# Optimization experiments

Hardware: AMD Instinct MI355X
Metric: run time of the kernel (lower is better)

The kernel has to match this reference:

```python
import jax, jax.numpy as jnp
import numpy as np

D_MODEL = 1024
NHEAD = 16
HEAD_DIM = D_MODEL // NHEAD
EPS = 1e-8


def setup_inputs() -> dict:
    key = jax.random.key(0)
    ks = jax.random.split(key, 10)
    B, T = 2, 2048
    s = 1.0 / np.sqrt(D_MODEL)
    return {
        "query": jax.random.normal(ks[0], (B, T, D_MODEL), jnp.float32),
        "key": jax.random.normal(ks[1], (B, T, D_MODEL), jnp.float32),
        "value": jax.random.normal(ks[2], (B, T, D_MODEL), jnp.float32),
        "frac": jax.random.uniform(ks[3], (B, T), jnp.float32),
        "Wq": jax.random.normal(ks[4], (D_MODEL, D_MODEL), jnp.float32) * s,
        "bq": jnp.zeros((D_MODEL,), jnp.float32),
        "Wk": jax.random.normal(ks[5], (D_MODEL, D_MODEL), jnp.float32) * s,
        "bk": jnp.zeros((D_MODEL,), jnp.float32),
        "Wv": jax.random.normal(ks[6], (D_MODEL, D_MODEL), jnp.float32) * s,
        "bv": jnp.zeros((D_MODEL,), jnp.float32),
        "attn_bias": jax.random.normal(ks[7], (HEAD_DIM,), jnp.float32) * 0.02,
        "Wo": jax.random.normal(ks[8], (D_MODEL, D_MODEL), jnp.float32) * s,
        "bo": jnpp if False else jnp.zeros((D_MODEL,), jnp.float32),
    }


def reference(query, key, value, frac, Wq, bq, Wk, bk, Wv, bv, attn_bias, Wo, bo):
    B, T, _ = query.shape
    H, Dh = NHEAD, HEAD_DIM
    scale = Dh ** -0.5

    # torch Linear: x @ W.T + b
    Q = (query @ Wq.T + bq).reshape(B, T, H, Dh).transpose(0, 2, 1, 3)  # [B,H,T,Dh]
    K = (key @ Wk.T + bk).reshape(B, T, H, Dh).transpose(0, 2, 1, 3)
    V = (value @ Wv.T + bv).reshape(B, T, H, Dh).transpose(0, 2, 1, 3)

    # factor_ij = (frac_j - frac_i) / (frac_i*frac_j + eps), shape [B,T,T]
    fi = frac[:, :, None]
    fj = frac[:, None, :]
    factor = (fj - fi) / (fi * fj + EPS)

    # sum_d (Q_i*K_j + attn_bias*factor)_d == QK^T + sum(attn_bias)*factor
    bias_sum = jnp.sum(attn_bias)
    logits = jnp.einsum('bhid,bhjd->bhij', Q, K) + bias_sum * factor[:, None, :, :]
    logits = logits * scale

    probs = jax.nn.softmax(logits, axis=-1)  # dropout p=0.0 (eval)
    out = jnp.einsum('bhij,bhjd->bhid', probs, V)  # [B,H,T,Dh]
    out = out.transpose(0, 2, 1, 3).reshape(B, T, H * Dh)
    return out @ Wo.T + bo
```

## Files before the change

kernel.cpp:

```cpp
#include <hip/hip_runtime.h>

typedef short s16x8 __attribute__((ext_vector_type(8)));
typedef float f32x4 __attribute__((ext_vector_type(4)));
typedef unsigned int u32x2 __attribute__((ext_vector_type(2)));
typedef unsigned short u16;
typedef unsigned int u32;

#define D_MODEL 1024
#define NHEAD   16
#define HD      64
#define TSEQ    2048
#define NB      2
#define MROWS   4096
#define NSPLIT  2
#define NTILES  (TSEQ / 64 / NSPLIT)

#define LOG2E 1.4426950408889634f
#define QSCALE (0.125f * LOG2E)

__device__ __forceinline__ u16 f2bf(float f) {
  unsigned u = __builtin_bit_cast(unsigned, f);
  u += 0x7fffu + ((u >> 16) & 1u);
  return (u16)(u >> 16);
}

__device__ __forceinline__ float bf2f(u16 x) {
  return __builtin_bit_cast(float, (u32)x << 16);
}

__device__ __forceinline__ u32 cvtpk(float lo, float hi) {
  u32 r;
  asm("v_cvt_pk_bf16_f32 %0, %1, %2" : "=v"(r) : "v"(lo), "v"(hi));
  return r;
}

__device__ __forceinline__ float exp2fast(float x) {
#if __has_builtin(__builtin_amdgcn_exp2f)
  return __builtin_amdgcn_exp2f(x);
#else
  return exp2f(x);
#endif
}

__device__ __forceinline__ float rcpfast(float x) {
#if __has_builtin(__builtin_amdgcn_rcpf)
  return __builtin_amdgcn_rcpf(x);
#else
  return 1.f / x;
#endif
}

__device__ __forceinline__ void gload16(const void* g, void* l) {
  __builtin_amdgcn_global_load_lds((const __attribute__((address_space(1))) void*)g,
                                   (__attribute__((address_space(3))) void*)l,
                                   16, 0, 0);
}

__global__ void cvt_all(const float* __restrict__ q, const float* __restrict__ k,
                        const float* __restrict__ v, const float* __restrict__ wq,
                        const float* __restrict__ wk, const float* __restrict__ wv,
                        const float* __restrict__ wo, const float* __restrict__ ab,
                        u16* qb, u16* kb, u16* vb, u16* wqb, u16* wkb, u16* wvb, u16* wob,
                        float* bsum) {
  if (blockIdx.x == 16384) {
    if (threadIdx.x < 64) {
      float s = ab[threadIdx.x];
#pragma unroll
      for (int m = 32; m >= 1; m >>= 1) s += __shfl_xor(s, m);
      if (threadIdx.x == 0) bsum[0] = s * 0.125f * LOG2E;
    }
    return;
  }
  int i = blockIdx.x * 256 + threadIdx.x;
  const float* src; u16* dst; int off;
  if (i < 3 * 1048576) {
    int t = i >> 20; off = i & 1048575;
    src = (t == 0) ? q : (t == 1) ? k : v;
    dst = (t == 0) ? qb : (t == 1) ? kb : vb;
  } else {
    int j = i - 3 * 1048576;
    int t = j >> 18; off = j & 262143;
    src = (t == 0) ? wq : (t == 1) ? wk : (t == 2) ? wv : wo;
    dst = (t == 0) ? wqb : (t == 1) ? wkb : (t == 2) ? wvb : wob;
  }
  float4 x = ((const float4*)src)[off];
  ushort4 o;
  o.x = f2bf(x.x); o.y = f2bf(x.y); o.z = f2bf(x.z); o.w = f2bf(x.w);
  ((ushort4*)dst)[off] = o;
}

template <int BM, int BN, int WN>
__device__ __forceinline__ void gemm_core(const u16* __restrict__ A, const u16* __restrict__ Bt,
                                          const float* __restrict__ bias, void* __restrict__ out,
                                          float oscale, int mode, u16* lds) {
  constexpr int K = 1024, N = 1024;
  constexpr int WM = 4 / WN;
  constexpr int WTM = BM / WM, WTN = BN / WN;
  constexpr int MR = WTM / 16, NR = WTN / 16;
  constexpr int ASZ = BM * 32, BSZ = BN * 32;
  constexpr int AISS = ASZ / 2048, BISS = BSZ / 2048;
  u16* lA = lds;
  u16* lB = lds + 2 * ASZ;

  const int tid = threadIdx.x;
  const int wid = tid >> 6, lane = tid & 63;
  const int l15 = lane & 15, lgp = lane >> 4;
  const int wr = wid / WN, wc = wid % WN;
  const int m0 = blockIdx.y * BM, n0 = blockIdx.x * BN;

  const u16* gA[AISS];
  const u16* gB[BISS];
#pragma unroll
  for (int i = 0; i < AISS; ++i) {
    int tp = i * 256 + tid, row = tp % BM, kc = tp / BM;
    gA[i] = A + (size_t)(m0 + row) * K + kc * 8;
  }
#pragma unroll
  for (int i = 0; i < BISS; ++i) {
    int tp = i * 256 + tid, row = tp % BN, kc = tp / BN;
    gB[i] = Bt + (size_t)(n0 + row) * K + kc * 8;
  }

  f32x4 acc[MR][NR];
#pragma unroll
  for (int m = 0; m < MR; ++m)
#pragma unroll
    for (int n = 0; n < NR; ++n) acc[m][n] = (f32x4){0.f, 0.f, 0.f, 0.f};

  auto stage = [&](int buf, int k0) {
#pragma unroll
    for (int i = 0; i < AISS; ++i)
      gload16(gA[i] + k0, lA + buf * ASZ + (i * 256 + tid) * 8);
#pragma unroll
    for (int i = 0; i < BISS; ++i)
      gload16(gB[i] + k0, lB + buf * BSZ + (i * 256 + tid) * 8);
  };

  int cur = 0;
  stage(0, 0);
  __syncthreads();
  for (int k0 = 0; k0 < K; k0 += 32) {
    if (k0 + 32 < K) stage(cur ^ 1, k0 + 32);
    const u16* a = lA + cur * ASZ;
    const u16* b = lB + cur * BSZ;
    s16x8 af[MR], bf[NR];
#pragma unroll
    for (int m = 0; m < MR; ++m)
      af[m] = *(const s16x8*)(a + lgp * BM * 8 + (wr * WTM + m * 16 + l15) * 8);
#pragma unroll
    for (int n = 0; n < NR; ++n)
      bf[n] = *(const s16x8*)(b + lgp * BN * 8 + (wc * WTN + n * 16 + l15) * 8);
    __builtin_amdgcn_s_setprio(1);
#pragma unroll
    for (int m = 0; m < MR; ++m)
#pragma unroll
      for (int n = 0; n < NR; ++n)
        acc[m][n] = __builtin_amdgcn_mfma_f32_16x16x32_bf16(af[m], bf[n], acc[m][n], 0, 0, 0);
    __builtin_amdgcn_s_setprio(0);
    __syncthreads();
    cur ^= 1;
  }

  float bvv[NR];
#pragma unroll
  for (int n = 0; n < NR; ++n) bvv[n] = bias[n0 + wc * WTN + n * 16 + l15];

#pragma unroll
  for (int m = 0; m < MR; ++m) {
    int rowb = m0 + wr * WTM + m * 16 + lgp * 4;
#pragma unroll
    for (int n = 0; n < NR; ++n) {
      int col = n0 + wc * WTN + n * 16 + l15;
#pragma unroll
      for (int r = 0; r < 4; ++r) {
        int row = rowb + r;
        float vv = (acc[m][n][r] + bvv[n]) * oscale;
        if (mode == 2) {
          ((float*)out)[(size_t)row * N + col] = vv;
        } else {
          int b = row >> 11, t = row & 2047;
          int h = col >> 6, d = col & 63;
          u16 x = f2bf(vv);
          if (mode == 0)
            ((u16*)out)[(((size_t)(b * NHEAD + h) * TSEQ + t) << 6) + d] = x;
          else
            ((u16*)out)[(((size_t)(b * NHEAD + h) * HD + d) << 11) + t] = x;
        }
      }
    }
  }
}

__global__ __launch_bounds__(256) void gemm_qkv(const u16* __restrict__ qb, const u16* __restrict__ kb,
                                                const u16* __restrict__ vb,
                                                const u16* __restrict__ Wqb, const u16* __restrict__ Wkb,
                                                const u16* __restrict__ Wvb,
                                                const float* __restrict__ bq, const float* __restrict__ bk,
                                                const float* __restrict__ bv,
                                                u16* Qp, u16* Kp, u16* Vtp) {
  __shared__ __align__(16) u16 lds[2 * 128 * 32 * 2];
  int z = blockIdx.z;
  const u16* A  = (z == 0) ? qb : (z == 1) ? kb : vb;
  const u16* Bt = (z == 0) ? Wqb : (z == 1) ? Wkb : Wvb;
  const float* bias = (z == 0) ? bq : (z == 1) ? bk : bv;
  u16* out = (z == 0) ? Qp : (z == 1) ? Kp : Vtp;
  int mode = (z == 2) ? 1 : 0;
  float oscale = (z == 0) ? QSCALE : 1.0f;
  gemm_core<128, 128, 2>(A, Bt, bias, out, oscale, mode, lds);
}

__global__ __launch_bounds__(256) void gemm_out(const u16* __restrict__ A, const u16* __restrict__ Bt,
                                                const float* __restrict__ bias, float* __restrict__ out) {
  __shared__ __align__(16) u16 lds[2 * 64 * 32 + 2 * 128 * 32];
  gemm_core<64, 128, 4>(A, Bt, bias, out, 1.0f, 2, lds);
}

__global__ __launch_bounds__(256, 4) void attn_kernel(const u16* __restrict__ Qp,
                                                      const u16* __restrict__ Kp,
                                                      const u16* __restrict__ Vt,
                                                      const float* __restrict__ frac,
                                                      const float* __restrict__ bsum,
                                                      u16* __restrict__ o0,
                                                      u16* __restrict__ o1,
                                                      float2* __restrict__ ml) {
  __shared__ __align__(16) u16 kbuf[64 * 64];
  __shared__ __align__(16) u16 vbuf[2][64 * 64];
  __shared__ __align__(16) u16 plds[4][16 * 64];
  const int tid = threadIdx.x, wid = tid >> 6, lane = tid & 63;
  const int l15 = lane & 15, lgp = lane >> 4;
  const int bh = blockIdx.y, b = bh >> 4, h = bh & 15;
  const int z = blockIdx.z;
  const int kvbase = z * (TSEQ / NSPLIT);
  u16* opart = z ? o1 : o0;
  float2* mlz = ml + z * (NB * NHEAD * TSEQ);
  const u16* Qh = Qp + (size_t)bh * TSEQ * HD;
  const u16* Kh = Kp + (size_t)bh * TSEQ * HD;
  const u16* Vh = Vt + (size_t)bh * HD * TSEQ;
  const float* fb = frac + b * TSEQ;
  const float bs = bsum[0];
  const float THR2 = 24.0f;
  const int q0 = blockIdx.x * 64 + wid * 16;

  const int srow = lane >> 3;
  const int sg8 = ((lane & 7) ^ srow) * 8;
  const int rbase = wid * 8 + srow;

  const int ofs0 = l15 * 64 + ((lgp ^ (l15 & 7)) * 8);
  const int ofs1 = l15 * 64 + (((4 + lgp) ^ (l15 & 7)) * 8);

  s16x8 qf[2];
#pragma unroll
  for (int ks = 0; ks < 2; ++ks)
    qf[ks] = *(const s16x8*)(Qh + (size_t)(q0 + l15) * HD + ks * 32 + lgp * 8);

  const float fi = fb[q0 + l15];
  const float nbfi = -bs * fi;
  float m2run = -1e30f;
  float lsum = 0.f;
  f32x4 o[4];
#pragma unroll
  for (int nd = 0; nd < 4; ++nd) o[nd] = (f32x4){0.f, 0.f, 0.f, 0.f};

  auto stageK = [&](int t) {
    int kv0s = kvbase + t * 64;
#pragma unroll
    for (int i = 0; i < 2; ++i)
      gload16(Kh + (size_t)(kv0s + i * 32 + rbase) * HD + sg8, &kbuf[i * 2048 + wid * 512]);
  };
  auto stageV = [&](int buf, int t) {
    int kv0s = kvbase + t * 64;
#pragma unroll
    for (int i = 0; i < 2; ++i)
      gload16(Vh + (size_t)(i * 32 + rbase) * TSEQ + kv0s + sg8, &vbuf[buf][i * 2048 + wid * 512]);
  };

  int cur = 0;
  stageK(0);
  stageV(0, 0);
  __syncthreads();

  for (int t = 0; t < NTILES; ++t) {
    s16x8 kf[4][2];
#pragma unroll
    for (int n = 0; n < 4; ++n) {
      kf[n][0] = *(const s16x8*)(&kbuf[0] + n * 1024 + ofs0);
      kf[n][1] = *(const s16x8*)(&kbuf[0] + n * 1024 + ofs1);
    }
    float4 fj4[4];
#pragma unroll
    for (int n = 0; n < 4; ++n)
      fj4[n] = *(const float4*)(fb + kvbase + t * 64 + n * 16 + lgp * 4);

    __syncthreads();
    if (t + 1 < NTILES) { stageK(t + 1); stageV(cur ^ 1, t + 1); }

    f32x4 s[4];
    __builtin_amdgcn_s_setprio(1);
#pragma unroll
    for (int n = 0; n < 4; ++n) {
      f32x4 a = (f32x4){0.f, 0.f, 0.f, 0.f};
      a = __builtin_amdgcn_mfma_f32_16x16x32_bf16(kf[n][0], qf[0], a, 0, 0, 0);
      a = __builtin_amdgcn_mfma_f32_16x16x32_bf16(kf[n][1], qf[1], a, 0, 0, 0);
      s[n] = a;
    }
    __builtin_amdgcn_s_setprio(0);

    float pmax = -1e30f;
#pragma unroll
    for (int n = 0; n < 4; ++n) {
#pragma unroll
      for (int r = 0; r < 4; ++r) {
        float fj = (r == 0) ? fj4[n].x : (r == 1) ? fj4[n].y : (r == 2) ? fj4[n].z : fj4[n].w;
        float num = __builtin_fmaf(bs, fj, nbfi);
        float den = __builtin_fmaf(fi, fj, 1e-8f);
        float l2 = __builtin_fmaf(num, rcpfast(den), s[n][r]);
        s[n][r] = l2;
        pmax = fmaxf(pmax, l2);
      }
    }

    if (__any((pmax - m2run) > THR2)) {
      float tm = fmaxf(pmax, __shfl_xor(pmax, 16));
      tm = fmaxf(tm, __shfl_xor(tm, 32));
      float m2n = fmaxf(m2run, tm);
      float alpha = exp2fast(m2run - m2n);
      lsum *= alpha;
      m2run = m2n;
      float af[4];
#pragma unroll
      for (int r = 0; r < 4; ++r) af[r] = __shfl(alpha, lgp * 4 + r);
#pragma unroll
      for (int nd = 0; nd < 4; ++nd)
#pragma unroll
        for (int r = 0; r < 4; ++r) o[nd][r] *= af[r];
    }

    u32 w[4][2];
    {
      float ps = 0.f;
#pragma unroll
      for (int n = 0; n < 4; ++n) {
#pragma unroll
        for (int s2 = 0; s2 < 2; ++s2) {
          float p0 = exp2fast(s[n][2 * s2 + 0] - m2run);
          float p1 = exp2fast(s[n][2 * s2 + 1] - m2run);
          ps += p0 + p1;
          w[n][s2] = cvtpk(p0, p1);
        }
      }
      lsum += ps;
    }

    u16* pw = &plds[wid][0];
#pragma unroll
    for (int n = 0; n < 4; ++n) {
      int idx = l15 * 64 + ((n * 16 + lgp * 4) ^ ((l15 & 7) << 3));
      *(u32x2*)(pw + idx) = (u32x2){w[n][0], w[n][1]};
    }
    s16x8 pf[2];
#pragma unroll
    for (int ks = 0; ks < 2; ++ks) {
      int idx = l15 * 64 + ((ks * 32 + lgp * 8) ^ ((l15 & 7) << 3));
      pf[ks] = *(const s16x8*)(pw + idx);
    }

    const u16* vbp = &vbuf[cur][0];
    __builtin_amdgcn_s_setprio(1);
#pragma unroll
    for (int nd = 0; nd < 4; ++nd) {
      s16x8 vf0 = *(const s16x8*)(vbp + nd * 1024 + ofs0);
      s16x8 vf1 = *(const s16x8*)(vbp + nd * 1024 + ofs1);
      o[nd] = __builtin_amdgcn_mfma_f32_16x16x32_bf16(pf[0], vf0, o[nd], 0, 0, 0);
      o[nd] = __builtin_amdgcn_mfma_f32_16x16x32_bf16(pf[1], vf1, o[nd], 0, 0, 0);
    }
    __builtin_amdgcn_s_setprio(0);

    __syncthreads();
    cur ^= 1;
  }

  {
    float l = lsum;
    l += __shfl_xor(l, 16);
    l += __shfl_xor(l, 32);
    if (lgp == 0)
      mlz[(bh << 11) + q0 + l15] = make_float2(m2run, l);
#pragma unroll
    for (int nd = 0; nd < 4; ++nd)
#pragma unroll
      for (int r = 0; r < 4; ++r) {
        int q = q0 + lgp * 4 + r;
        opart[((size_t)(b * TSEQ + q)) * D_MODEL + h * HD + nd * 16 + l15] = f2bf(o[nd][r]);
      }
  }
}

__global__ __launch_bounds__(256) void attn_combine(const u16* __restrict__ o0,
                                                    const u16* __restrict__ o1,
                                                    const float2* __restrict__ ml,
                                                    u16* __restrict__ aout) {
  int g = blockIdx.x * 256 + threadIdx.x;
  int bth = g >> 3, j0 = (g & 7) * 8;
  int b = bth >> 15, t = (bth >> 4) & 2047, h = bth & 15;
  int mlidx = (((b << 4) | h) << 11) | t;
  float2 v0 = ml[mlidx];
  float2 v1 = ml[NB * NHEAD * TSEQ + mlidx];
  float M = fmaxf(v0.x, v1.x);
  float a0 = exp2fast(v0.x - M), a1 = exp2fast(v1.x - M);
  float rd = __fdividef(1.f, __builtin_fmaf(v0.y, a0, v1.y * a1));
  float s0 = a0 * rd, s1 = a1 * rd;
  size_t base = (size_t)bth * 64 + j0;
  s16x8 x0 = *(const s16x8*)(o0 + base);
  s16x8 x1 = *(const s16x8*)(o1 + base);
  s16x8 out;
#pragma unroll
  for (int j = 0; j < 8; ++j) {
    float f = __builtin_fmaf(bf2f((u16)x0[j]), s0, bf2f((u16)x1[j]) * s1);
    out[j] = (short)f2bf(f);
  }
  *(s16x8*)(aout + base) = out;
}

extern "C" void kernel_launch(void* const* d_in, const int* in_sizes, int n_in,
                              void* d_out, int out_size, void* d_ws, size_t ws_size,
                              hipStream_t stream) {
  const float* query = (const float*)d_in[0];
  const float* key_  = (const float*)d_in[1];
  const float* value = (const float*)d_in[2];
  const float* frac  = (const float*)d_in[3];
  const float* Wq    = (const float*)d_in[4];
  const float* bq    = (const float*)d_in[5];
  const float* Wk    = (const float*)d_in[6];
  const float* bk    = (const float*)d_in[7];
  const float* Wv    = (const float*)d_in[8];
  const float* bv    = (const float*)d_in[9];
  const float* abias = (const float*)d_in[10];
  const float* Wo    = (const float*)d_in[11];
  const float* bo    = (const float*)d_in[12];

  char* ws = (char*)d_ws;
  size_t off = 0;
  auto alloc = [&](size_t bytes) { char* p = ws + off; off += (bytes + 255) & ~255ULL; return p; };
  const size_t XB = (size_t)MROWS * D_MODEL * 2;
  const size_t WB = (size_t)D_MODEL * D_MODEL * 2;
  u16* qb  = (u16*)alloc(XB);
  u16* kb  = (u16*)alloc(XB);
  u16* vb  = (u16*)alloc(XB);
  u16* Wqb = (u16*)alloc(WB);
  u16* Wkb = (u16*)alloc(WB);
  u16* Wvb = (u16*)alloc(WB);
  u16* Wob = (u16*)alloc(WB);
  float* bsum = (float*)alloc(256);
  u16* Qp  = (u16*)alloc(XB);
  u16* Kp  = (u16*)alloc(XB);
  u16* Vtp = (u16*)alloc(XB);
  u16* AO  = (u16*)alloc(XB);

  u16* o0 = qb;
  u16* o1 = kb;
  float2* ml = (float2*)vb;

  cvt_all<<<dim3(16385), dim3(256), 0, stream>>>(query, key_, value, Wq, Wk, Wv, Wo, abias,
                                                 qb, kb, vb, Wqb, Wkb, Wvb, Wob, bsum);

  gemm_qkv<<<dim3(D_MODEL / 128, MROWS / 128, 3), dim3(256), 0, stream>>>(
      qb, kb, vb, Wqb, Wkb, Wvb, bq, bk, bv, Qp, Kp, Vtp);

  attn_kernel<<<dim3(TSEQ / 64, NB * NHEAD, NSPLIT), dim3(256), 0, stream>>>(
      Qp, Kp, Vtp, frac, bsum, o0, o1, ml);

  attn_combine<<<dim3(MROWS * D_MODEL / 8 / 256), dim3(256), 0, stream>>>(o0, o1, ml, AO);

  gemm_out<<<dim3(D_MODEL / 128, MROWS / 64), dim3(256), 0, stream>>>(AO, Wob, bo, (float*)d_out);
}
```

Baseline: 187.4 us.

## Enlarge attention blocks to 8 waves and transpose V-projection MFMA for coalesced stores

The attention kernel now runs 512 threads per block covering 128 query rows, so each K/V tile staged in LDS is shared by twice as many waves and total K/V traffic drops. Each thread now issues a single staging load per tile instead of two. The GEMM core gains a compile-time MODE. For the V projection it swaps MFMA operands so each lane holds consecutive token positions, which makes the transposed Vt stores contiguous in t rather than strided. The risks are higher register and LDS pressure per block, fewer blocks in flight for attention, and a changed store pattern.

```diff
diff --git a/kernel.cpp b/kernel.cpp
--- a/kernel.cpp
+++ b/kernel.cpp
@@ -89,10 +89,10 @@
   ((ushort4*)dst)[off] = o;
 }
 
-template <int BM, int BN, int WN>
+template <int BM, int BN, int WN, int MODE>
 __device__ __forceinline__ void gemm_core(const u16* __restrict__ A, const u16* __restrict__ Bt,
                                           const float* __restrict__ bias, void* __restrict__ out,
-                                          float oscale, int mode, u16* lds) {
+                                          float oscale, u16* lds) {
   constexpr int K = 1024, N = 1024;
   constexpr int WM = 4 / WN;
   constexpr int WTM = BM / WM, WTN = BN / WN;
@@ -154,37 +154,58 @@
 #pragma unroll
     for (int m = 0; m < MR; ++m)
 #pragma unroll
-      for (int n = 0; n < NR; ++n)
-        acc[m][n] = __builtin_amdgcn_mfma_f32_16x16x32_bf16(af[m], bf[n], acc[m][n], 0, 0, 0);
+      for (int n = 0; n < NR; ++n) {
+        if (MODE == 1)
+          acc[m][n] = __builtin_amdgcn_mfma_f32_16x16x32_bf16(bf[n], af[m], acc[m][n], 0, 0, 0);
+        else
+          acc[m][n] = __builtin_amdgcn_mfma_f32_16x16x32_bf16(af[m], bf[n], acc[m][n], 0, 0, 0);
+      }
     __builtin_amdgcn_s_setprio(0);
     __syncthreads();
     cur ^= 1;
   }
 
-  float bvv[NR];
-#pragma unroll
-  for (int n = 0; n < NR; ++n) bvv[n] = bias[n0 + wc * WTN + n * 16 + l15];
-
-#pragma unroll
-  for (int m = 0; m < MR; ++m) {
-    int rowb = m0 + wr * WTM + m * 16 + lgp * 4;
-#pragma unroll
-    for (int n = 0; n < NR; ++n) {
-      int col = n0 + wc * WTN + n * 16 + l15;
-#pragma unroll
-      for (int r = 0; r < 4; ++r) {
-        int row = rowb + r;
-        float vv = (acc[m][n][r] + bvv[n]) * oscale;
-        if (mode == 2) {
-          ((float*)out)[(size_t)row * N + col] = vv;
-        } else {
-          int b = row >> 11, t = row & 2047;
-          int h = col >> 6, d = col & 63;
-          u16 x = f2bf(vv);
-          if (mode == 0)
-            ((u16*)out)[(((size_t)(b * NHEAD + h) * TSEQ + t) << 6) + d] = x;
-          else
-            ((u16*)out)[(((size_t)(b * NHEAD + h) * HD + d) << 11) + t] = x;
+  if (MODE == 1) {
+    float4 bvv4[NR];
+#pragma unroll
+    for (int n = 0; n < NR; ++n)
+      bvv4[n] = *(const float4*)(bias + n0 + wc * WTN + n * 16 + lgp * 4);
+#pragma unroll
+    for (int m = 0; m < MR; ++m) {
+      int m_abs = m0 + wr * WTM + m * 16 + l15;
+      int bb = m_abs >> 11, t = m_abs & 2047;
+#pragma unroll
+      for (int n = 0; n < NR; ++n) {
+#pragma unroll
+        for (int r = 0; r < 4; ++r) {
+          int n_abs = n0 + wc * WTN + n * 16 + lgp * 4 + r;
+          int h = n_abs >> 6, d = n_abs & 63;
+          float vv = (acc[m][n][r] + ((const float*)&bvv4[n])[r]) * oscale;
+          ((u16*)out)[(((size_t)((bb * NHEAD + h) * HD + d)) << 11) + t] = f2bf(vv);
+        }
+      }
+    }
+  } else {
+    float bvv[NR];
+#pragma unroll
+    for (int n = 0; n < NR; ++n) bvv[n] = bias[n0 + wc * WTN + n * 16 + l15];
+#pragma unroll
+    for (int m = 0; m < MR; ++m) {
+      int rowb = m0 + wr * WTM + m * 16 + lgp * 4;
+#pragma unroll
+      for (int n = 0; n < NR; ++n) {
+        int col = n0 + wc * WTN + n * 16 + l15;
+#pragma unroll
+        for (int r = 0; r < 4; ++r) {
+          int row = rowb + r;
+          float vv = (acc[m][n][r] + bvv[n]) * oscale;
+          if (MODE == 2) {
+            ((float*)out)[(size_t)row * N + col] = vv;
+          } else {
+            int b = row >> 11, t = row & 2047;
+            int h = col >> 6, d = col & 63;
+            ((u16*)out)[(((size_t)(b * NHEAD + h) * TSEQ + t) << 6) + d] = f2bf(vv);
+          }
         }
       }
     }
@@ -200,22 +221,21 @@
                                                 u16* Qp, u16* Kp, u16* Vtp) {
   __shared__ __align__(16) u16 lds[2 * 128 * 32 * 2];
   int z = blockIdx.z;
-  const u16* A  = (z == 0) ? qb : (z == 1) ? kb : vb;
-  const u16* Bt = (z == 0) ? Wqb : (z == 1) ? Wkb : Wvb;
-  const float* bias = (z == 0) ? bq : (z == 1) ? bk : bv;
-  u16* out = (z == 0) ? Qp : (z == 1) ? Kp : Vtp;
-  int mode = (z == 2) ? 1 : 0;
-  float oscale = (z == 0) ? QSCALE : 1.0f;
-  gemm_core<128, 128, 2>(A, Bt, bias, out, oscale, mode, lds);
+  if (z == 0)
+    gemm_core<128, 128, 2, 0>(qb, Wqb, bq, Qp, QSCALE, lds);
+  else if (z == 1)
+    gemm_core<128, 128, 2, 0>(kb, Wkb, bk, Kp, 1.0f, lds);
+  else
+    gemm_core<128, 128, 2, 1>(vb, Wvb, bv, Vtp, 1.0f, lds);
 }
 
 __global__ __launch_bounds__(256) void gemm_out(const u16* __restrict__ A, const u16* __restrict__ Bt,
                                                 const float* __restrict__ bias, float* __restrict__ out) {
   __shared__ __align__(16) u16 lds[2 * 64 * 32 + 2 * 128 * 32];
-  gemm_core<64, 128, 4>(A, Bt, bias, out, 1.0f, 2, lds);
-}
-
-__global__ __launch_bounds__(256, 4) void attn_kernel(const u16* __restrict__ Qp,
+  gemm_core<64, 128, 4, 2>(A, Bt, bias, out, 1.0f, lds);
+}
+
+__global__ __launch_bounds__(512, 8) void attn_kernel(const u16* __restrict__ Qp,
                                                       const u16* __restrict__ Kp,
                                                       const u16* __restrict__ Vt,
                                                       const float* __restrict__ frac,
@@ -225,7 +245,7 @@
                                                       float2* __restrict__ ml) {
   __shared__ __align__(16) u16 kbuf[64 * 64];
   __shared__ __align__(16) u16 vbuf[2][64 * 64];
-  __shared__ __align__(16) u16 plds[4][16 * 64];
+  __shared__ __align__(16) u16 plds[8][16 * 64];
   const int tid = threadIdx.x, wid = tid >> 6, lane = tid & 63;
   const int l15 = lane & 15, lgp = lane >> 4;
   const int bh = blockIdx.y, b = bh >> 4, h = bh & 15;
@@ -239,7 +259,7 @@
   const float* fb = frac + b * TSEQ;
   const float bs = bsum[0];
   const float THR2 = 24.0f;
-  const int q0 = blockIdx.x * 64 + wid * 16;
+  const int q0 = blockIdx.x * 128 + wid * 16;
 
   const int srow = lane >> 3;
   const int sg8 = ((lane & 7) ^ srow) * 8;
@@ -263,15 +283,11 @@
 
   auto stageK = [&](int t) {
     int kv0s = kvbase + t * 64;
-#pragma unroll
-    for (int i = 0; i < 2; ++i)
-      gload16(Kh + (size_t)(kv0s + i * 32 + rbase) * HD + sg8, &kbuf[i * 2048 + wid * 512]);
+    gload16(Kh + (size_t)(kv0s + rbase) * HD + sg8, &kbuf[wid * 512]);
   };
   auto stageV = [&](int buf, int t) {
     int kv0s = kvbase + t * 64;
-#pragma unroll
-    for (int i = 0; i < 2; ++i)
-      gload16(Vh + (size_t)(i * 32 + rbase) * TSEQ + kv0s + sg8, &vbuf[buf][i * 2048 + wid * 512]);
+    gload16(Vh + (size_t)rbase * TSEQ + kv0s + sg8, &vbuf[buf][wid * 512]);
   };
 
   int cur = 0;
@@ -466,7 +482,7 @@
   gemm_qkv<<<dim3(D_MODEL / 128, MROWS / 128, 3), dim3(256), 0, stream>>>(
       qb, kb, vb, Wqb, Wkb, Wvb, bq, bk, bv, Qp, Kp, Vtp);
 
-  attn_kernel<<<dim3(TSEQ / 64, NB * NHEAD, NSPLIT), dim3(256), 0, stream>>>(
+  attn_kernel<<<dim3(TSEQ / 128, NB * NHEAD, NSPLIT), dim3(512), 0, stream>>>(
       Qp, Kp, Vtp, frac, bsum, o0, o1, ml);
 
   attn_combine<<<dim3(MROWS * D_MODEL / 8 / 256), dim3(256), 0, stream>>>(o0, o1, ml, AO);
```

New measurement: 612.1 us. +226.7%, slower.
